# Kernel tuning notes

Measured on AMD Instinct MI355X. Metric: run time of the kernel, lower is better.

## Reference

```python
import jax, jax.numpy as jnp
import numpy as np
import math

N_QUBITS = 8
N_QLAYERS = 1
LN_EPS = 1e-5


def _rx(state, theta, wire, n):
    # state: (N, 2,...,2) complex64 with n qubit axes; theta: (N,)
    sh = (theta.shape[0],) + (1,) * (n - 1)
    c = jnp.cos(theta / 2).reshape(sh)
    s = jnp.sin(theta / 2).reshape(sh)
    a = jax.lax.index_in_dim(state, 0, wire + 1, keepdims=False)
    b = jax.lax.index_in_dim(state, 1, wire + 1, keepdims=False)
    return jnp.stack([c * a - 1j * s * b, -1j * s * a + c * b], axis=wire + 1)


def _cnot(state, cw, tw, n):
    s0 = jax.lax.index_in_dim(state, 0, cw + 1, keepdims=False)
    s1 = jax.lax.index_in_dim(state, 1, cw + 1, keepdims=False)
    t_ax = tw + 1 if tw < cw else tw  # target axis index after removing control axis
    s1 = jnp.flip(s1, axis=t_ax)
    return jnp.stack([s0, s1], axis=cw + 1)


def _quantum(angles, qweights):
    # AngleEmbedding (RX) + BasicEntanglerLayers (RX + CNOT ring) + PauliZ expvals
    # angles: (N, 8) float; qweights: (1, 8) float -> returns (N, 8) float
    n = N_QUBITS
    N = angles.shape[0]
    state = jnp.zeros((N,) + (2,) * n, jnp.complex64)
    state = state.at[(slice(None),) + (0,) * n].set(1.0 + 0j)
    for w in range(n):
        state = _rx(state, angles[:, w], w, n)
    for l in range(N_QLAYERS):
        for w in range(n):
            state = _rx(state, jnp.broadcast_to(qweights[l, w], (N,)), w, n)
        for cw in range(n):
            state = _cnot(state, cw, (cw + 1) % n, n)
    probs = state.real ** 2 + state.imag ** 2
    zs = []
    for w in range(n):
        p = probs.sum(axis=tuple(a for a in range(1, n + 1) if a != w + 1))  # (N, 2)
        zs.append(p[:, 0] - p[:, 1])
    return jnp.stack(zs, axis=-1)


def _layernorm(x, g, b):
    m = x.mean(-1, keepdims=True)
    v = ((x - m) ** 2).mean(-1, keepdims=True)
    return (x - m) / jnp.sqrt(v + LN_EPS) * g + b


def _forward(x, Wq, Wk, Wv, Wo, ln1_g, ln1_b, W1, b1, W2, b2, ln2_g, ln2_b,
             ql1_w, ql1_b, qweights, ql2_w, ql2_b):
    B, S, D = x.shape
    H = 16
    dk = D // H
    q = (x @ Wq.T).reshape(B, S, H, dk)
    k = (x @ Wk.T).reshape(B, S, H, dk)
    v = (x @ Wv.T).reshape(B, S, H, dk)
    scores = jnp.einsum('bqhd,bkhd->bhqk', q, k) * (1.0 / math.sqrt(dk))
    attn = jax.nn.softmax(scores, axis=-1)
    o = jnp.einsum('bhqk,bkhd->bqhd', attn, v).reshape(B, S, D) @ Wo.T
    x = _layernorm(o + x, ln1_g, ln1_b)
    ff = jax.nn.relu(x @ W1.T + b1) @ W2.T + b2
    x = _layernorm(ff + x, ln2_g, ln2_b)
    angles = (x @ ql1_w.T + ql1_b).reshape(B * S, N_QUBITS)
    z = _quantum(angles, qweights).reshape(B, S, N_QUBITS).astype(x.dtype)
    y = jnp.concatenate([z, x], axis=2) @ ql2_w.T + ql2_b
    return y


def setup_inputs() -> dict:
    key = jax.random.key(0)
    ks = jax.random.split(key, 12)
    B, S, D, F = 4, 1024, 1024, 4096
    sc = 0.02
    w = lambda k, *sh: jax.random.normal(k, sh, jnp.float32) * sc
    return {
        'x': jax.random.normal(ks[0], (B, S, D), jnp.float32),
        'Wq': w(ks[1], D, D), 'Wk': w(ks[2], D, D), 'Wv': w(ks[3], D, D), 'Wo': w(ks[4], D, D),
        'ln1_g': jnp.ones((D,), jnp.float32), 'ln1_b': jnp.zeros((D,), jnp.float32),
        'W1': w(ks[5], F, D), 'b1': jnp.zeros((F,), jnp.float32),
        'W2': w(ks[6], D, F), 'b2': jnp.zeros((D,), jnp.float32),
        'ln2_g': jnp.ones((D,), jnp.float32), 'ln2_b': jnp.zeros((D,), jnp.float32),
        'ql1_w': w(ks[7], N_QUBITS, D), 'ql1_b': jnp.zeros((N_QUBITS,), jnp.float32),
        'qweights': jax.random.uniform(ks[8], (N_QLAYERS, N_QUBITS), jnp.float32, 0.0, 2 * np.pi),
        'ql2_w': w(ks[9], D, D + N_QUBITS), 'ql2_b': jnp.zeros((D,), jnp.float32),
    }


def reference(x, Wq, Wk, Wv, Wo, ln1_g, ln1_b, W1, b1, W2, b2, ln2_g, ln2_b,
              ql1_w, ql1_b, qweights, ql2_w, ql2_b):
    return _forward(x, Wq, Wk, Wv, Wo, ln1_g, ln1_b, W1, b1, W2, b2, ln2_g, ln2_b,
                    ql1_w, ql1_b, qweights, ql2_w, ql2_b)
```

## Files before the change

kernel.cpp:

```cpp
#include <hip/hip_runtime.h>
#include <hip/hip_bf16.h>

typedef __bf16 bf16_t;
typedef __attribute__((ext_vector_type(8))) __bf16 bf16x8;
typedef __attribute__((ext_vector_type(4))) float floatx4;

#define BM 128

enum { EPI_NONE = 0, EPI_RESID, EPI_BIAS_RELU, EPI_BIAS_RESID, EPI_QL2 };

__device__ __forceinline__ void gld_lds16(const bf16_t* g, bf16_t* l) {
  __builtin_amdgcn_global_load_lds(
      (__attribute__((address_space(1))) void*)(g),
      (__attribute__((address_space(3))) void*)(l), 16, 0, 0);
}

template<int ROWS, int COLS>
__device__ __forceinline__ void stage_swz(const bf16_t* g, int ld, bf16_t* lds, int tid) {
  constexpr int G = COLS / 8;
  #pragma unroll
  for (int i = 0; i < ROWS * G / 256; ++i) {
    int ci = i * 256 + tid;
    int row = ci / G, cc = ci % G;
    int gg = (G == 8) ? (cc ^ (row & 7)) : ((cc & 8) | ((cc & 7) ^ (row & 7)));
    gld_lds16(g + (size_t)row * ld + gg * 8, lds + ci * 8);
  }
}

__device__ __forceinline__ void core128(const bf16_t* __restrict__ Ag,
                                        const bf16_t* __restrict__ Bg,
                                        int K, int ldb,
                                        bf16_t* As, bf16_t* Bs,
                                        floatx4 acc[4][4]) {
  const int tid = threadIdx.x;
  const int wid = tid >> 6, lane = tid & 63;
  const int wm = (wid >> 1) * 64, wn = (wid & 1) * 64;
  const int m16 = lane & 15, quad = lane >> 4;
  const int r7 = m16 & 7;
  for (int k0 = 0; k0 < K; k0 += 64) {
    stage_swz<128, 64>(Ag + k0, K, As, tid);
    stage_swz<128, 64>(Bg + k0, ldb, Bs, tid);
    __syncthreads();
    #pragma unroll
    for (int ks = 0; ks < 2; ++ks) {
      const int gi = ks * 4 + quad;
      const int slot = gi ^ r7;
      bf16x8 af[4], bfr[4];
      #pragma unroll
      for (int mt = 0; mt < 4; ++mt)
        af[mt] = *(const bf16x8*)&As[((wm + mt * 16 + m16) * 8 + slot) * 8];
      #pragma unroll
      for (int nt = 0; nt < 4; ++nt)
        bfr[nt] = *(const bf16x8*)&Bs[((wn + nt * 16 + m16) * 8 + slot) * 8];
      #pragma unroll
      for (int mt = 0; mt < 4; ++mt)
        #pragma unroll
        for (int nt = 0; nt < 4; ++nt)
          acc[mt][nt] = __builtin_amdgcn_mfma_f32_16x16x32_bf16(af[mt], bfr[nt], acc[mt][nt], 0, 0, 0);
    }
    __syncthreads();
  }
}

template<int EPI>
__global__ __launch_bounds__(256)
void gemm128(const bf16_t* __restrict__ A, const bf16_t* __restrict__ B,
             bf16_t* __restrict__ C, const float* __restrict__ bias,
             int N, int K) {
  __shared__ bf16_t As[BM * 64];
  __shared__ bf16_t Bs[BM * 64];
  const int tid = threadIdx.x;
  const int wid = tid >> 6, lane = tid & 63;
  const int wm = (wid >> 1) * 64, wn = (wid & 1) * 64;
  const int m16 = lane & 15, quad = lane >> 4;
  const int m0 = blockIdx.y * BM, n0 = blockIdx.x * BM;
  floatx4 acc[4][4];
  const floatx4 vzero = {0.f, 0.f, 0.f, 0.f};
  #pragma unroll
  for (int mt = 0; mt < 4; ++mt)
    #pragma unroll
    for (int nt = 0; nt < 4; ++nt) acc[mt][nt] = vzero;
  core128(A + (size_t)m0 * K, B + (size_t)n0 * K, K, K, As, Bs, acc);
  #pragma unroll
  for (int mt = 0; mt < 4; ++mt)
    #pragma unroll
    for (int nt = 0; nt < 4; ++nt) {
      const int gcol = n0 + wn + nt * 16 + m16;
      float bv = (EPI == EPI_BIAS_RELU) ? bias[gcol] : 0.f;
      #pragma unroll
      for (int r = 0; r < 4; ++r) {
        const int grow = m0 + wm + mt * 16 + quad * 4 + r;
        float v = acc[mt][nt][r];
        if (EPI == EPI_BIAS_RELU) { v += bv; v = fmaxf(v, 0.f); }
        C[(size_t)grow * N + gcol] = (bf16_t)v;
      }
    }
}

__global__ __launch_bounds__(256)
void gemm_qkv(const bf16_t* __restrict__ X, const bf16_t* __restrict__ Wb,
              bf16_t* __restrict__ Qo, bf16_t* __restrict__ Ko, bf16_t* __restrict__ Vt) {
  __shared__ bf16_t As[BM * 64];
  __shared__ bf16_t Bs[BM * 64];
  const int tid = threadIdx.x;
  const int wid = tid >> 6, lane = tid & 63;
  const int wm = (wid >> 1) * 64, wn = (wid & 1) * 64;
  const int m16 = lane & 15, quad = lane >> 4;
  const int m0 = blockIdx.y * BM, n0 = blockIdx.x * BM;
  const int sel = blockIdx.z;
  const bf16_t* B = Wb + (size_t)sel * 1024 * 1024;
  floatx4 acc[4][4];
  const floatx4 vzero = {0.f, 0.f, 0.f, 0.f};
  #pragma unroll
  for (int mt = 0; mt < 4; ++mt)
    #pragma unroll
    for (int nt = 0; nt < 4; ++nt) acc[mt][nt] = vzero;
  core128(X + (size_t)m0 * 1024, B + (size_t)n0 * 1024, 1024, 1024, As, Bs, acc);
  if (sel < 2) {
    bf16_t* C = sel ? Ko : Qo;
    const float sc = sel ? 1.f : 0.125f;
    #pragma unroll
    for (int mt = 0; mt < 4; ++mt)
      #pragma unroll
      for (int nt = 0; nt < 4; ++nt) {
        const int gcol = n0 + wn + nt * 16 + m16;
        #pragma unroll
        for (int r = 0; r < 4; ++r) {
          const int grow = m0 + wm + mt * 16 + quad * 4 + r;
          C[(size_t)grow * 1024 + gcol] = (bf16_t)(acc[mt][nt][r] * sc);
        }
      }
  } else {
    #pragma unroll
    for (int mt = 0; mt < 4; ++mt) {
      const int grow0 = m0 + wm + mt * 16 + quad * 4;
      const int b = grow0 >> 10, s = grow0 & 1023;
      #pragma unroll
      for (int nt = 0; nt < 4; ++nt) {
        const int gcol = n0 + wn + nt * 16 + m16;
        const int h = gcol >> 6, d = gcol & 63;
        #pragma unroll
        for (int r = 0; r < 4; ++r)
          Vt[(((size_t)b * 16 + h) * 64 + d) * 1024 + s + r] = (bf16_t)acc[mt][nt][r];
      }
    }
  }
}

template<int EPI, bool OUTF32>
__global__ __launch_bounds__(256)
void gemm64(const bf16_t* __restrict__ A, const bf16_t* __restrict__ B,
            void* __restrict__ Cv,
            const bf16_t* __restrict__ resid, const float* __restrict__ bias,
            const bf16_t* __restrict__ z, const float* __restrict__ zw,
            int N, int K, int ldb, int boff) {
  __shared__ bf16_t As[BM * 128];
  __shared__ bf16_t Bs[64 * 128];
  const int tid = threadIdx.x;
  const int wid = tid >> 6, lane = tid & 63;
  const int wm = (wid >> 1) * 64, wn = (wid & 1) * 32;
  const int m16 = lane & 15, quad = lane >> 4;
  const int r7 = m16 & 7;
  const int m0 = blockIdx.y * BM, n0 = blockIdx.x * 64;
  const bf16_t* Ag = A + (size_t)m0 * K;
  const bf16_t* Bg = B + (size_t)n0 * ldb + boff;
  floatx4 acc[4][2];
  const floatx4 vzero = {0.f, 0.f, 0.f, 0.f};
  #pragma unroll
  for (int mt = 0; mt < 4; ++mt)
    #pragma unroll
    for (int nt = 0; nt < 2; ++nt) acc[mt][nt] = vzero;
  for (int k0 = 0; k0 < K; k0 += 128) {
    stage_swz<128, 128>(Ag + k0, K, As, tid);
    stage_swz<64, 128>(Bg + k0, ldb, Bs, tid);
    __syncthreads();
    #pragma unroll
    for (int ks = 0; ks < 4; ++ks) {
      const int gi = ks * 4 + quad;
      const int slot = (gi & 8) | ((gi & 7) ^ r7);
      bf16x8 af[4], bfr[2];
      #pragma unroll
      for (int mt = 0; mt < 4; ++mt)
        af[mt] = *(const bf16x8*)&As[((wm + mt * 16 + m16) * 16 + slot) * 8];
      #pragma unroll
      for (int nt = 0; nt < 2; ++nt)
        bfr[nt] = *(const bf16x8*)&Bs[((wn + nt * 16 + m16) * 16 + slot) * 8];
      #pragma unroll
      for (int mt = 0; mt < 4; ++mt)
        #pragma unroll
        for (int nt = 0; nt < 2; ++nt)
          acc[mt][nt] = __builtin_amdgcn_mfma_f32_16x16x32_bf16(af[mt], bfr[nt], acc[mt][nt], 0, 0, 0);
    }
    __syncthreads();
  }
  #pragma unroll
  for (int mt = 0; mt < 4; ++mt)
    #pragma unroll
    for (int nt = 0; nt < 2; ++nt) {
      const int gcol = n0 + wn + nt * 16 + m16;
      float bv = 0.f;
      if (EPI == EPI_BIAS_RESID || EPI == EPI_QL2) bv = bias[gcol];
      #pragma unroll
      for (int r = 0; r < 4; ++r) {
        const int grow = m0 + wm + mt * 16 + quad * 4 + r;
        float v = acc[mt][nt][r];
        if (EPI == EPI_RESID) v += (float)resid[(size_t)grow * N + gcol];
        if (EPI == EPI_BIAS_RESID) v += bv + (float)resid[(size_t)grow * N + gcol];
        if (EPI == EPI_QL2) {
          float s = 0.f;
          #pragma unroll
          for (int u = 0; u < 8; ++u)
            s += (float)z[(size_t)grow * 8 + u] * zw[(size_t)gcol * 1032 + u];
          v += bv + s;
        }
        if (OUTF32) ((float*)Cv)[(size_t)grow * N + gcol] = v;
        else        ((bf16_t*)Cv)[(size_t)grow * N + gcol] = (bf16_t)v;
      }
    }
}

__global__ __launch_bounds__(256)
void attn_kernel(const bf16_t* __restrict__ Q, const bf16_t* __restrict__ Kb,
                 const bf16_t* __restrict__ Vt, bf16_t* __restrict__ O) {
  __shared__ bf16_t Qs[64 * 64];
  __shared__ bf16_t Ks[128 * 64];
  __shared__ bf16_t Vs[64 * 128];
  __shared__ bf16_t Ps[4][16 * 128];
  const int tid = threadIdx.x;
  const int wid = tid >> 6, lane = tid & 63;
  const int m16 = lane & 15, quad = lane >> 4;
  const int qt = blockIdx.x, bh = blockIdx.y;
  const int b = bh >> 4, h = bh & 15;
  const size_t qbase = ((size_t)(b * 1024 + qt * 64)) * 1024 + h * 64;
  #pragma unroll
  for (int i = 0; i < 2; ++i) {
    int ci = i * 256 + tid;
    int row = ci >> 3, cc = ci & 7;
    *(bf16x8*)&Qs[row * 64 + ((cc ^ (row & 7)) * 8)] =
        *(const bf16x8*)&Q[qbase + (size_t)row * 1024 + cc * 8];
  }
  __syncthreads();
  const int qm = wid * 16 + m16;
  bf16x8 qf0 = *(const bf16x8*)&Qs[qm * 64 + ((quad ^ (qm & 7)) * 8)];
  bf16x8 qf1 = *(const bf16x8*)&Qs[qm * 64 + (((4 + quad) ^ (qm & 7)) * 8)];
  floatx4 oacc[4];
  float rs[4];
  const floatx4 vzero = {0.f, 0.f, 0.f, 0.f};
  #pragma unroll
  for (int dt = 0; dt < 4; ++dt) oacc[dt] = vzero;
  #pragma unroll
  for (int r = 0; r < 4; ++r) rs[r] = 0.f;
  const size_t kbase = ((size_t)(b * 1024)) * 1024 + h * 64;
  const size_t vbase = ((size_t)bh * 64) * 1024;
  for (int kt = 0; kt < 8; ++kt) {
    __syncthreads();
    #pragma unroll
    for (int i = 0; i < 4; ++i) {
      int ci = i * 256 + tid;
      int row = ci >> 3, cc = ci & 7;
      *(bf16x8*)&Ks[row * 64 + ((cc ^ (row & 7)) * 8)] =
          *(const bf16x8*)&Kb[kbase + (size_t)(kt * 128 + row) * 1024 + cc * 8];
    }
    #pragma unroll
    for (int i = 0; i < 4; ++i) {
      int ci = i * 256 + tid;
      int dr = ci >> 4, cc = ci & 15;
      int gs = (cc & 8) | ((cc & 7) ^ (dr & 7));
      *(bf16x8*)&Vs[dr * 128 + gs * 8] =
          *(const bf16x8*)&Vt[vbase + (size_t)dr * 1024 + kt * 128 + cc * 8];
    }
    __syncthreads();
    floatx4 sa[8];
    #pragma unroll
    for (int nt = 0; nt < 8; ++nt) sa[nt] = vzero;
    #pragma unroll
    for (int nt = 0; nt < 8; ++nt) {
      const int n = nt * 16 + m16;
      bf16x8 kf0 = *(const bf16x8*)&Ks[n * 64 + ((quad ^ (n & 7)) * 8)];
      bf16x8 kf1 = *(const bf16x8*)&Ks[n * 64 + (((4 + quad) ^ (n & 7)) * 8)];
      sa[nt] = __builtin_amdgcn_mfma_f32_16x16x32_bf16(qf0, kf0, sa[nt], 0, 0, 0);
      sa[nt] = __builtin_amdgcn_mfma_f32_16x16x32_bf16(qf1, kf1, sa[nt], 0, 0, 0);
    }
    #pragma unroll
    for (int nt = 0; nt < 8; ++nt)
      #pragma unroll
      for (int r = 0; r < 4; ++r) {
        float pv = __expf(sa[nt][r]);
        rs[r] += pv;
        const int prow = quad * 4 + r;
        const int g = nt * 2 + (m16 >> 3);
        const int gs = (g & 8) | ((g & 7) ^ (prow & 7));
        Ps[wid][prow * 128 + gs * 8 + (m16 & 7)] = (bf16_t)pv;
      }
    bf16x8 pf[4];
    #pragma unroll
    for (int ksub = 0; ksub < 4; ++ksub) {
      const int g = ksub * 4 + quad;
      const int gs = (g & 8) | ((g & 7) ^ (m16 & 7));
      pf[ksub] = *(const bf16x8*)&Ps[wid][m16 * 128 + gs * 8];
    }
    #pragma unroll
    for (int dt = 0; dt < 4; ++dt) {
      const int n = dt * 16 + m16;
      #pragma unroll
      for (int ksub = 0; ksub < 4; ++ksub) {
        const int g = ksub * 4 + quad;
        const int gs = (g & 8) | ((g & 7) ^ (n & 7));
        bf16x8 vf = *(const bf16x8*)&Vs[n * 128 + gs * 8];
        oacc[dt] = __builtin_amdgcn_mfma_f32_16x16x32_bf16(pf[ksub], vf, oacc[dt], 0, 0, 0);
      }
    }
  }
  #pragma unroll
  for (int r = 0; r < 4; ++r) {
    rs[r] += __shfl_xor(rs[r], 1);
    rs[r] += __shfl_xor(rs[r], 2);
    rs[r] += __shfl_xor(rs[r], 4);
    rs[r] += __shfl_xor(rs[r], 8);
  }
  const size_t obase = ((size_t)(b * 1024 + qt * 64 + wid * 16)) * 1024 + h * 64;
  #pragma unroll
  for (int dt = 0; dt < 4; ++dt)
    #pragma unroll
    for (int r = 0; r < 4; ++r)
      O[obase + (size_t)(quad * 4 + r) * 1024 + dt * 16 + m16] = (bf16_t)(oacc[dt][r] / rs[r]);
}

struct Segs {
  const float* s[5];
  bf16_t* d[5];
  int n8[5];
};
__global__ __launch_bounds__(256)
void conv_multi(Segs sg) {
  const int zz = blockIdx.z;
  const float* in = sg.s[zz];
  bf16_t* out = sg.d[zz];
  const int n8 = sg.n8[zz];
  for (int i = blockIdx.x * 256 + threadIdx.x; i < n8; i += gridDim.x * 256) {
    const float* p = in + (size_t)i * 8;
    floatx4 a = *(const floatx4*)p;
    floatx4 b = *(const floatx4*)(p + 4);
    bf16x8 o;
    #pragma unroll
    for (int j = 0; j < 4; ++j) { o[j] = (bf16_t)a[j]; o[4 + j] = (bf16_t)b[j]; }
    *(bf16x8*)(out + (size_t)i * 8) = o;
  }
}

__global__ __launch_bounds__(256)
void ln_kernel(const bf16_t* __restrict__ in, const float* __restrict__ g,
               const float* __restrict__ b, bf16_t* __restrict__ out) {
  const int row = blockIdx.x * 4 + (threadIdx.x >> 6);
  const int lane = threadIdx.x & 63;
  const bf16_t* p = in + (size_t)row * 1024 + lane * 16;
  bf16x8 v0 = *(const bf16x8*)p;
  bf16x8 v1 = *(const bf16x8*)(p + 8);
  float f[16];
  #pragma unroll
  for (int j = 0; j < 8; ++j) { f[j] = (float)v0[j]; f[8 + j] = (float)v1[j]; }
  float s = 0.f, ss = 0.f;
  #pragma unroll
  for (int j = 0; j < 16; ++j) { s += f[j]; ss += f[j] * f[j]; }
  #pragma unroll
  for (int off = 1; off < 64; off <<= 1) { s += __shfl_xor(s, off); ss += __shfl_xor(ss, off); }
  const float m = s * (1.f / 1024.f);
  const float inv_sd = rsqrtf(ss * (1.f / 1024.f) - m * m + 1e-5f);
  const float* gp = g + lane * 16;
  const float* bp = b + lane * 16;
  bf16x8 o0, o1;
  #pragma unroll
  for (int j = 0; j < 8; ++j) o0[j] = (bf16_t)((f[j] - m) * inv_sd * gp[j] + bp[j]);
  #pragma unroll
  for (int j = 0; j < 8; ++j) o1[j] = (bf16_t)((f[8 + j] - m) * inv_sd * gp[8 + j] + bp[8 + j]);
  *(bf16x8*)&out[(size_t)row * 1024 + lane * 16] = o0;
  *(bf16x8*)&out[(size_t)row * 1024 + lane * 16 + 8] = o1;
}

__global__ __launch_bounds__(256)
void quantum_kernel(const bf16_t* __restrict__ x2, const float* __restrict__ qw1,
                    const float* __restrict__ qb1, const float* __restrict__ qwt,
                    bf16_t* __restrict__ z) {
  const int row = blockIdx.x * 4 + (threadIdx.x >> 6);
  const int lane = threadIdx.x & 63;
  const bf16_t* xp = x2 + (size_t)row * 1024 + lane * 16;
  bf16x8 xv0 = *(const bf16x8*)xp;
  bf16x8 xv1 = *(const bf16x8*)(xp + 8);
  float th[8];
  #pragma unroll
  for (int qq = 0; qq < 8; ++qq) {
    const float* wp = qw1 + (size_t)qq * 1024 + lane * 16;
    float s = 0.f;
    #pragma unroll
    for (int j = 0; j < 8; ++j) s += (float)xv0[j] * wp[j] + (float)xv1[j] * wp[8 + j];
    #pragma unroll
    for (int off = 1; off < 64; off <<= 1) s += __shfl_xor(s, off);
    th[qq] = s + qb1[qq] + qwt[qq];
  }
  if (lane == 0) {
    float c[8];
    #pragma unroll
    for (int qq = 0; qq < 8; ++qq) c[qq] = cosf(th[qq]);
    float z0 = 1.f;
    #pragma unroll
    for (int u = 1; u < 8; ++u) z0 *= c[u];
    z[(size_t)row * 8 + 0] = (bf16_t)z0;
    float p = c[0];
    #pragma unroll
    for (int w = 1; w < 8; ++w) { p *= c[w]; z[(size_t)row * 8 + w] = (bf16_t)p; }
  }
}

extern "C" void kernel_launch(void* const* d_in, const int* in_sizes, int n_in,
                              void* d_out, int out_size, void* d_ws, size_t ws_size,
                              hipStream_t stream) {
  const float* x    = (const float*)d_in[0];
  const float* Wq   = (const float*)d_in[1];
  const float* Wk   = (const float*)d_in[2];
  const float* Wv   = (const float*)d_in[3];
  const float* Wo   = (const float*)d_in[4];
  const float* ln1g = (const float*)d_in[5];
  const float* ln1b = (const float*)d_in[6];
  const float* W1   = (const float*)d_in[7];
  const float* b1   = (const float*)d_in[8];
  const float* W2   = (const float*)d_in[9];
  const float* b2   = (const float*)d_in[10];
  const float* ln2g = (const float*)d_in[11];
  const float* ln2b = (const float*)d_in[12];
  const float* qw1  = (const float*)d_in[13];
  const float* qb1  = (const float*)d_in[14];
  const float* qwt  = (const float*)d_in[15];
  const float* ql2w = (const float*)d_in[16];
  const float* ql2b = (const float*)d_in[17];
  bf16_t* ws = (bf16_t*)d_ws;

  const size_t T = (size_t)4096 * 1024;
  const size_t M1 = (size_t)1024 * 1024;
  bf16_t* outlo = (bf16_t*)d_out;
  bf16_t* outhi = outlo + T;

  bf16_t* xb    = ws;
  bf16_t* kb    = ws + T;
  bf16_t* vt    = ws + 2 * T;
  bf16_t* ff    = ws + 3 * T;
  bf16_t* wqkvb = ff;
  bf16_t* wob   = ff + 3 * M1;
  bf16_t* w1b   = vt;
  bf16_t* w2b   = kb;
  bf16_t* ql2wb = vt;
  bf16_t* q     = outlo;
  bf16_t* o     = outhi;
  bf16_t* x1p   = outlo;
  bf16_t* x1    = outhi;
  bf16_t* x2p   = outlo;
  bf16_t* x2    = xb;
  bf16_t* z     = kb;

  {
    Segs sg;
    sg.s[0] = x;  sg.d[0] = xb;            sg.n8[0] = (int)(T / 8);
    sg.s[1] = Wq; sg.d[1] = wqkvb;         sg.n8[1] = (int)(M1 / 8);
    sg.s[2] = Wk; sg.d[2] = wqkvb + M1;    sg.n8[2] = (int)(M1 / 8);
    sg.s[3] = Wv; sg.d[3] = wqkvb + 2*M1;  sg.n8[3] = (int)(M1 / 8);
    sg.s[4] = Wo; sg.d[4] = wob;           sg.n8[4] = (int)(M1 / 8);
    conv_multi<<<dim3(512, 1, 5), 256, 0, stream>>>(sg);
  }
  gemm_qkv<<<dim3(8, 32, 3), 256, 0, stream>>>(xb, wqkvb, q, kb, vt);
  attn_kernel<<<dim3(16, 64), 256, 0, stream>>>(q, kb, vt, o);
  gemm64<EPI_RESID, false><<<dim3(16, 32), 256, 0, stream>>>(
      o, wob, x1p, xb, nullptr, nullptr, nullptr, 1024, 1024, 1024, 0);
  ln_kernel<<<1024, 256, 0, stream>>>(x1p, ln1g, ln1b, x1);
  {
    Segs sg;
    sg.s[0] = W1; sg.d[0] = w1b; sg.n8[0] = (int)(T / 8);
    sg.s[1] = W2; sg.d[1] = w2b; sg.n8[1] = (int)(T / 8);
    sg.s[2] = nullptr; sg.d[2] = nullptr; sg.n8[2] = 0;
    sg.s[3] = nullptr; sg.d[3] = nullptr; sg.n8[3] = 0;
    sg.s[4] = nullptr; sg.d[4] = nullptr; sg.n8[4] = 0;
    conv_multi<<<dim3(1024, 1, 2), 256, 0, stream>>>(sg);
  }
  gemm128<EPI_BIAS_RELU><<<dim3(32, 32), 256, 0, stream>>>(x1, w1b, ff, b1, 4096, 1024);
  gemm64<EPI_BIAS_RESID, false><<<dim3(16, 32), 256, 0, stream>>>(
      ff, w2b, x2p, x1, b2, nullptr, nullptr, 1024, 4096, 4096, 0);
  ln_kernel<<<1024, 256, 0, stream>>>(x2p, ln2g, ln2b, x2);
  quantum_kernel<<<1024, 256, 0, stream>>>(x2, qw1, qb1, qwt, z);
  {
    Segs sg;
    sg.s[0] = ql2w; sg.d[0] = ql2wb; sg.n8[0] = 1024 * 1032 / 8;
    sg.s[1] = nullptr; sg.d[1] = nullptr; sg.n8[1] = 0;
    sg.s[2] = nullptr; sg.d[2] = nullptr; sg.n8[2] = 0;
    sg.s[3] = nullptr; sg.d[3] = nullptr; sg.n8[3] = 0;
    sg.s[4] = nullptr; sg.d[4] = nullptr; sg.n8[4] = 0;
    conv_multi<<<dim3(512, 1, 1), 256, 0, stream>>>(sg);
  }
  gemm64<EPI_QL2, true><<<dim3(16, 32), 256, 0, stream>>>(
      x2, ql2wb, d_out, nullptr, ql2b, z, ql2w, 1024, 1024, 1032, 8);
}
```

Measured before the change: 409.1 us.

## Fuse LN2 with quantum layer and ql2 weight conversion; remap gemm64 block order

Merges the second layernorm, the quantum expectation kernel and the ql2 weight fp32-to-bf16 conversion into one launch. The conversion runs in the z=1 slice, and the quantum dot products reuse the normalized values already held in registers, so x2 is not reread. This removes two kernel launches and one pass over x2. gemm64 now uses a 1D grid with M-fastest block ordering, so consecutive blocks share the same weight tile, which should improve L2 reuse of B.

```diff
diff --git a/kernel.cpp b/kernel.cpp
--- a/kernel.cpp
+++ b/kernel.cpp
@@ -153,7 +153,7 @@
             void* __restrict__ Cv,
             const bf16_t* __restrict__ resid, const float* __restrict__ bias,
             const bf16_t* __restrict__ z, const float* __restrict__ zw,
-            int N, int K, int ldb, int boff) {
+            int N, int K, int ldb, int boff, int mblocks) {
   __shared__ bf16_t As[BM * 128];
   __shared__ bf16_t Bs[64 * 128];
   const int tid = threadIdx.x;
@@ -161,7 +161,8 @@
   const int wm = (wid >> 1) * 64, wn = (wid & 1) * 32;
   const int m16 = lane & 15, quad = lane >> 4;
   const int r7 = m16 & 7;
-  const int m0 = blockIdx.y * BM, n0 = blockIdx.x * 64;
+  const int id = blockIdx.x;
+  const int m0 = (id % mblocks) * BM, n0 = (id / mblocks) * 64;
   const bf16_t* Ag = A + (size_t)m0 * K;
   const bf16_t* Bg = B + (size_t)n0 * ldb + boff;
   floatx4 acc[4][2];
@@ -378,24 +379,59 @@
 }
 
 __global__ __launch_bounds__(256)
-void quantum_kernel(const bf16_t* __restrict__ x2, const float* __restrict__ qw1,
-                    const float* __restrict__ qb1, const float* __restrict__ qwt,
-                    bf16_t* __restrict__ z) {
+void ln2_quantum(const bf16_t* __restrict__ in, const float* __restrict__ g,
+                 const float* __restrict__ b, bf16_t* __restrict__ x2,
+                 const float* __restrict__ qw1, const float* __restrict__ qb1,
+                 const float* __restrict__ qwt, bf16_t* __restrict__ zout,
+                 const float* __restrict__ ql2w, bf16_t* __restrict__ ql2wb) {
+  if (blockIdx.z == 1) {
+    const int n8 = 1024 * 1032 / 8;
+    for (int i = blockIdx.x * 256 + threadIdx.x; i < n8; i += gridDim.x * 256) {
+      const float* p = ql2w + (size_t)i * 8;
+      floatx4 a = *(const floatx4*)p;
+      floatx4 bb = *(const floatx4*)(p + 4);
+      bf16x8 o;
+      #pragma unroll
+      for (int j = 0; j < 4; ++j) { o[j] = (bf16_t)a[j]; o[4 + j] = (bf16_t)bb[j]; }
+      *(bf16x8*)(ql2wb + (size_t)i * 8) = o;
+    }
+    return;
+  }
   const int row = blockIdx.x * 4 + (threadIdx.x >> 6);
   const int lane = threadIdx.x & 63;
-  const bf16_t* xp = x2 + (size_t)row * 1024 + lane * 16;
-  bf16x8 xv0 = *(const bf16x8*)xp;
-  bf16x8 xv1 = *(const bf16x8*)(xp + 8);
+  const bf16_t* p = in + (size_t)row * 1024 + lane * 16;
+  bf16x8 v0 = *(const bf16x8*)p;
+  bf16x8 v1 = *(const bf16x8*)(p + 8);
+  float f[16];
+  #pragma unroll
+  for (int j = 0; j < 8; ++j) { f[j] = (float)v0[j]; f[8 + j] = (float)v1[j]; }
+  float s = 0.f, ss = 0.f;
+  #pragma unroll
+  for (int j = 0; j < 16; ++j) { s += f[j]; ss += f[j] * f[j]; }
+  #pragma unroll
+  for (int off = 1; off < 64; off <<= 1) { s += __shfl_xor(s, off); ss += __shfl_xor(ss, off); }
+  const float m = s * (1.f / 1024.f);
+  const float inv_sd = rsqrtf(ss * (1.f / 1024.f) - m * m + 1e-5f);
+  const float* gp = g + lane * 16;
+  const float* bp = b + lane * 16;
+  bf16x8 o0, o1;
+  #pragma unroll
+  for (int j = 0; j < 8; ++j) o0[j] = (bf16_t)((f[j] - m) * inv_sd * gp[j] + bp[j]);
+  #pragma unroll
+  for (int j = 0; j < 8; ++j) o1[j] = (bf16_t)((f[8 + j] - m) * inv_sd * gp[8 + j] + bp[8 + j]);
+  *(bf16x8*)&x2[(size_t)row * 1024 + lane * 16] = o0;
+  *(bf16x8*)&x2[(size_t)row * 1024 + lane * 16 + 8] = o1;
   float th[8];
   #pragma unroll
   for (int qq = 0; qq < 8; ++qq) {
     const float* wp = qw1 + (size_t)qq * 1024 + lane * 16;
-    float s = 0.f;
-    #pragma unroll
-    for (int j = 0; j < 8; ++j) s += (float)xv0[j] * wp[j] + (float)xv1[j] * wp[8 + j];
-    #pragma unroll
-    for (int off = 1; off < 64; off <<= 1) s += __shfl_xor(s, off);
-    th[qq] = s + qb1[qq] + qwt[qq];
+    float sdot = 0.f;
+    #pragma unroll
+    for (int j = 0; j < 8; ++j)
+      sdot += (float)o0[j] * wp[j] + (float)o1[j] * wp[8 + j];
+    #pragma unroll
+    for (int off = 1; off < 64; off <<= 1) sdot += __shfl_xor(sdot, off);
+    th[qq] = sdot + qb1[qq] + qwt[qq];
   }
   if (lane == 0) {
     float c[8];
@@ -404,10 +440,10 @@
     float z0 = 1.f;
     #pragma unroll
     for (int u = 1; u < 8; ++u) z0 *= c[u];
-    z[(size_t)row * 8 + 0] = (bf16_t)z0;
-    float p = c[0];
-    #pragma unroll
-    for (int w = 1; w < 8; ++w) { p *= c[w]; z[(size_t)row * 8 + w] = (bf16_t)p; }
+    zout[(size_t)row * 8 + 0] = (bf16_t)z0;
+    float pp = c[0];
+    #pragma unroll
+    for (int w = 1; w < 8; ++w) { pp *= c[w]; zout[(size_t)row * 8 + w] = (bf16_t)pp; }
   }
 }
 
@@ -467,8 +503,8 @@
   }
   gemm_qkv<<<dim3(8, 32, 3), 256, 0, stream>>>(xb, wqkvb, q, kb, vt);
   attn_kernel<<<dim3(16, 64), 256, 0, stream>>>(q, kb, vt, o);
-  gemm64<EPI_RESID, false><<<dim3(16, 32), 256, 0, stream>>>(
-      o, wob, x1p, xb, nullptr, nullptr, nullptr, 1024, 1024, 1024, 0);
+  gemm64<EPI_RESID, false><<<512, 256, 0, stream>>>(
+      o, wob, x1p, xb, nullptr, nullptr, nullptr, 1024, 1024, 1024, 0, 32);
   ln_kernel<<<1024, 256, 0, stream>>>(x1p, ln1g, ln1b, x1);
   {
     Segs sg;
@@ -480,19 +516,10 @@
     conv_multi<<<dim3(1024, 1, 2), 256, 0, stream>>>(sg);
   }
   gemm128<EPI_BIAS_RELU><<<dim3(32, 32), 256, 0, stream>>>(x1, w1b, ff, b1, 4096, 1024);
-  gemm64<EPI_BIAS_RESID, false><<<dim3(16, 32), 256, 0, stream>>>(
-      ff, w2b, x2p, x1, b2, nullptr, nullptr, 1024, 4096, 4096, 0);
-  ln_kernel<<<1024, 256, 0, stream>>>(x2p, ln2g, ln2b, x2);
-  quantum_kernel<<<1024, 256, 0, stream>>>(x2, qw1, qb1, qwt, z);
-  {
-    Segs sg;
-    sg.s[0] = ql2w; sg.d[0] = ql2wb; sg.n8[0] = 1024 * 1032 / 8;
-    sg.s[1] = nullptr; sg.d[1] = nullptr; sg.n8[1] = 0;
-    sg.s[2] = nullptr; sg.d[2] = nullptr; sg.n8[2] = 0;
-    sg.s[3] = nullptr; sg.d[3] = nullptr; sg.n8[3] = 0;
-    sg.s[4] = nullptr; sg.d[4] = nullptr; sg.n8[4] = 0;
-    conv_multi<<<dim3(512, 1, 1), 256, 0, stream>>>(sg);
-  }
-  gemm64<EPI_QL2, true><<<dim3(16, 32), 256, 0, stream>>>(
-      x2, ql2wb, d_out, nullptr, ql2b, z, ql2w, 1024, 1024, 1032, 8);
-}
+  gemm64<EPI_BIAS_RESID, false><<<512, 256, 0, stream>>>(
+      ff, w2b, x2p, x1, b2, nullptr, nullptr, 1024, 4096, 4096, 0, 32);
+  ln2_quantum<<<dim3(1024, 1, 2), 256, 0, stream>>>(
+      x2p, ln2g, ln2b, x2, qw1, qb1, qwt, z, ql2w, ql2wb);
+  gemm64<EPI_QL2, true><<<512, 256, 0, stream>>>(
+      x2, ql2wb, d_out, nullptr, ql2b, z, ql2w, 1024, 1024, 1032, 8, 32);
+}
```

New measurement: 400.6 us. -2.1%, faster.
